# Performance work log

Hardware: AMD Instinct MI355X
Metric: run time of the kernel (lower is better)

Reference implementation:

```python
import jax, jax.numpy as jnp
import numpy as np
import math

# Equal-size graphs make SAGPooling's top-k static; removed edges are kept with a validity mask.
B, N0, D, H, HID, POS, DEG = 64, 400, 128, 4, 64, 16, 16
C = D // H                     # per-head dim = 32
EG = N0 * DEG                  # edges per graph
E = B * EG                     # 409600 edges total
RATIO = 0.8
K1 = math.ceil(RATIO * N0)     # 320
K2 = math.ceil(RATIO * K1)     # 256
K3 = math.ceil(RATIO * K2)     # 205
KS = (K1, K2, K3)
EPS = 1e-5

def _lin(x, W, b):
    return x @ W + b

def _ln(x, g, b):
    mu = x.mean(-1, keepdims=True)
    var = ((x - mu) ** 2).mean(-1, keepdims=True)
    return (x - mu) * jax.lax.rsqrt(var + EPS) * g + b

def _bn(x, g, b):  # BatchNorm1d, training mode (biased batch variance)
    mu = x.mean(0)
    var = ((x - mu) ** 2).mean(0)
    return (x - mu) * jax.lax.rsqrt(var + EPS) * g + b

def _transformer_conv(x, src, dst, mask, Wq, bq, Wk, bk, Wv, bv, Ws, bs, N):
    # PyG TransformerConv (concat=True, root_weight=True): scatter-softmax attention over edges
    q = _lin(x, Wq, bq).reshape(N, H, C)
    k = _lin(x, Wk, bk).reshape(N, H, C)
    v = _lin(x, Wv, bv).reshape(N, H, C)
    logits = jnp.einsum('ehc,ehc->eh', q[dst], k[src]) / jnp.sqrt(jnp.float32(C))
    logits = jnp.where(mask[:, None], logits, -1e9)
    m = jnp.maximum(jax.ops.segment_max(logits, dst, num_segments=N), -1e9)
    w = jnp.exp(logits - m[dst]) * mask[:, None]
    denom = jax.ops.segment_sum(w, dst, num_segments=N)
    alpha = w / jnp.where(denom[dst] > 0, denom[dst], 1.0)  # [E,H]
    msg = jax.ops.segment_sum(v[src] * alpha[:, :, None], dst, num_segments=N)
    return msg.reshape(N, D) + _lin(x, Ws, bs)

def _gt_block(x, src, dst, mask, Wq, bq, Wk, bk, Wv, bv, Ws, bs,
              Wlo, blo, g1, be1, W1, b1, W2, b2, g2, be2, N):
    out1 = _lin(_transformer_conv(x, src, dst, mask, Wq, bq, Wk, bk, Wv, bv, Ws, bs, N), Wlo, blo)
    out2 = _ln(out1 + x, g1, be1)
    out3 = _lin(jax.nn.relu(_lin(out2, W1, b1)), W2, b2)
    return _ln(out3 + out2, g2, be2)

def _sag_pool(x, src, dst, mask, Wrel, brel, Wroot, n, k):
    # SAGPooling: GraphConv(aggr='add') scorer, tanh nonlinearity, per-graph top-k, filter_adj via mask
    Nn = B * n
    agg = jax.ops.segment_sum(x[src] * mask[:, None], dst, num_segments=Nn)
    s = jnp.tanh((agg @ Wrel + brel + x @ Wroot)[:, 0])
    tv, ti = jax.lax.top_k(s.reshape(B, n), k)  # [B,k]
    perm = (ti + jnp.arange(B, dtype=ti.dtype)[:, None] * n).reshape(-1)
    x_new = x[perm] * tv.reshape(-1, 1)
    kept = jnp.zeros(Nn, bool).at[perm].set(True)
    new_id = jnp.zeros(Nn, jnp.int32).at[perm].set(jnp.arange(B * k, dtype=jnp.int32))
    nm = mask & kept[src] & kept[dst]
    return x_new, jnp.where(nm, new_id[src], 0), jnp.where(nm, new_id[dst], 0), nm

def _forward(x, lap_pos_enc, W_pos, b_pos,
             gt_Wq, gt_bq, gt_Wk, gt_bk, gt_Wv, gt_bv, gt_Wskip, gt_bskip,
             gt_Wlo, gt_blo, gt_ln1g, gt_ln1b, gt_W1, gt_b1, gt_W2, gt_b2, gt_ln2g, gt_ln2b,
             pool_Wrel, pool_brel, pool_Wroot,
             hW1, hb1, hW2, hb2, hW3, hb3, bn1g, bn1b, bn2g, bn2b,
             edge_src, edge_dst):
    x = x + _lin(lap_pos_enc, W_pos, b_pos)
    src, dst = edge_src, edge_dst
    mask = jnp.ones(src.shape, bool)
    n = N0
    feats = []
    for i in range(3):
        x = _gt_block(x, src, dst, mask,
                      gt_Wq[i], gt_bq[i], gt_Wk[i], gt_bk[i], gt_Wv[i], gt_bv[i],
                      gt_Wskip[i], gt_bskip[i], gt_Wlo[i], gt_blo[i],
                      gt_ln1g[i], gt_ln1b[i], gt_W1[i], gt_b1[i], gt_W2[i], gt_b2[i],
                      gt_ln2g[i], gt_ln2b[i], B * n)
        x, src, dst, mask = _sag_pool(x, src, dst, mask, pool_Wrel[i], pool_brel[i], pool_Wroot[i], n, KS[i])
        n = KS[i]
        xg = x.reshape(B, n, D)
        feats.append(jnp.concatenate([xg.max(1), xg.mean(1)], axis=1))  # [B, 2D] = gmp | gap
    xf = feats[0] + feats[1] + feats[2]
    h = jax.nn.relu(_bn(_lin(xf, hW1, hb1), bn1g, bn1b))
    h = jax.nn.relu(_bn(_lin(h, hW2, hb2), bn2g, bn2b))
    return _lin(h, hW3, hb3)[:, 0]  # [B]

def setup_inputs():
    key = jax.random.key(0)
    ks = jax.random.split(key, 16)
    rn = lambda k, shape, fan: jax.random.normal(k, shape, jnp.float32) / np.float32(np.sqrt(fan))
    inp = {}
    inp['x'] = jax.random.normal(ks[0], (B * N0, D), jnp.float32)
    inp['lap_pos_enc'] = jax.random.normal(ks[1], (B * N0, POS), jnp.float32)
    offs = (jnp.arange(B, dtype=jnp.int32) * N0)[:, None]
    inp['edge_src'] = (jax.random.randint(ks[2], (B, EG), 0, N0, jnp.int32) + offs).reshape(-1)
    inp['edge_dst'] = (jax.random.randint(ks[3], (B, EG), 0, N0, jnp.int32) + offs).reshape(-1)
    inp['W_pos'] = rn(ks[4], (POS, D), POS); inp['b_pos'] = jnp.zeros(D)
    pk = jax.random.split(ks[5], 12)
    inp['gt_Wq'] = rn(pk[0], (3, D, D), D); inp['gt_bq'] = jnp.zeros((3, D))
    inp['gt_Wk'] = rn(pk[1], (3, D, D), D); inp['gt_bk'] = jnp.zeros((3, D))
    inp['gt_Wv'] = rn(pk[2], (3, D, D), D); inp['gt_bv'] = jnp.zeros((3, D))
    inp['gt_Wskip'] = rn(pk[3], (3, D, D), D); inp['gt_bskip'] = jnp.zeros((3, D))
    inp['gt_Wlo'] = rn(pk[4], (3, D, D), D); inp['gt_blo'] = jnp.zeros((3, D))
    inp['gt_ln1g'] = jnp.ones((3, D)); inp['gt_ln1b'] = jnp.zeros((3, D))
    inp['gt_W1'] = rn(pk[5], (3, D, HID), D); inp['gt_b1'] = jnp.zeros((3, HID))
    inp['gt_W2'] = rn(pk[6], (3, HID, D), HID); inp['gt_b2'] = jnp.zeros((3, D))
    inp['gt_ln2g'] = jnp.ones((3, D)); inp['gt_ln2b'] = jnp.zeros((3, D))
    inp['pool_Wrel'] = rn(pk[7], (3, D, 1), D); inp['pool_brel'] = jnp.zeros((3, 1))
    inp['pool_Wroot'] = rn(pk[8], (3, D, 1), D)
    inp['hW1'] = rn(pk[9], (2 * D, D), 2 * D); inp['hb1'] = jnp.zeros(D)
    inp['hW2'] = rn(pk[10], (D, D // 2), D); inp['hb2'] = jnp.zeros(D // 2)
    inp['hW3'] = rn(pk[11], (D // 2, 1), D // 2); inp['hb3'] = jnp.zeros(1)
    inp['bn1g'] = jnp.ones(D); inp['bn1b'] = jnp.zeros(D)
    inp['bn2g'] = jnp.ones(D // 2); inp['bn2b'] = jnp.zeros(D // 2)
    return inp

def reference(x, lap_pos_enc, edge_src, edge_dst, W_pos, b_pos,
              gt_Wq, gt_bq, gt_Wk, gt_bk, gt_Wv, gt_bv, gt_Wskip, gt_bskip,
              gt_Wlo, gt_blo, gt_ln1g, gt_ln1b, gt_W1, gt_b1, gt_W2, gt_b2, gt_ln2g, gt_ln2b,
              pool_Wrel, pool_brel, pool_Wroot,
              hW1, hb1, hW2, hb2, hW3, hb3, bn1g, bn1b, bn2g, bn2b):
    return _forward(x, lap_pos_enc, W_pos, b_pos,
                    gt_Wq, gt_bq, gt_Wk, gt_bk, gt_Wv, gt_bv, gt_Wskip, gt_bskip,
                    gt_Wlo, gt_blo, gt_ln1g, gt_ln1b, gt_W1, gt_b1, gt_W2, gt_b2, gt_ln2g, gt_ln2b,
                    pool_Wrel, pool_brel, pool_Wroot,
                    hW1, hb1, hW2, hb2, hW3, hb3, bn1g, bn1b, bn2g, bn2b,
                    edge_src, edge_dst)
```

## Files before the change

### kernel.cpp

```cpp
#include <hip/hip_runtime.h>
#include <math.h>

#define BB   64
#define NPG0 400
#define DD   128
#define HH   4
#define CC   32
#define HIDD 64
#define POSD 16
#define EE   409600
#define EG   6400

__global__ void k_pos(const float* __restrict__ x, const float* __restrict__ lap,
                      const float* __restrict__ Wp, const float* __restrict__ bp,
                      float* __restrict__ out, int N){
  __shared__ float W[POSD*DD];
  __shared__ float bsh[DD];
  for(int i=threadIdx.x;i<POSD*DD;i+=blockDim.x) W[i]=Wp[i];
  for(int i=threadIdx.x;i<DD;i+=blockDim.x) bsh[i]=bp[i];
  __syncthreads();
  int total=N*DD;
  for(int idx=blockIdx.x*blockDim.x+threadIdx.x; idx<total; idx+=gridDim.x*blockDim.x){
    int n=idx>>7, d=idx&127;
    const float* lr=lap+(size_t)n*POSD;
    float acc=bsh[d]+x[idx];
    #pragma unroll
    for(int p=0;p<POSD;p++) acc=fmaf(lr[p],W[p*DD+d],acc);
    out[idx]=acc;
  }
}

__global__ __launch_bounds__(512) void k_gemm4_sw(
    const float* __restrict__ X,
    const float* __restrict__ W0,const float* __restrict__ W1,
    const float* __restrict__ W2,const float* __restrict__ W3,
    const float* __restrict__ b0,const float* __restrict__ b1,
    const float* __restrict__ b2,const float* __restrict__ b3,
    float* __restrict__ Y0,float* __restrict__ Y1,
    float* __restrict__ Y2,float* __restrict__ Y3){
  constexpr int XPAD=DD+4;
  __shared__ float Xl[128*XPAD];
  int tid=threadIdx.x;
  { const float4* xs=(const float4*)(X+(size_t)blockIdx.x*128*DD);
    for(int i=tid;i<128*32;i+=512){
      int r=i>>5, kq=i&31;
      *(float4*)&Xl[r*XPAD+kq*4]=xs[i];
    } }
  __syncthreads();
  int lane=tid&63;
  int wv=__builtin_amdgcn_readfirstlane(tid>>6);
  int cbase=wv*16;
  int row0=blockIdx.x*128+lane;
  int row1=row0+64;
  const float* xr0=&Xl[lane*XPAD];
  const float* xr1=&Xl[(lane+64)*XPAD];
  auto one=[&](const float* __restrict__ Wg,const float* __restrict__ bias,float* __restrict__ Y){
    float a0[16],a1[16];
    #pragma unroll
    for(int c=0;c<16;c++){a0[c]=0.f;a1[c]=0.f;}
    #pragma unroll 2
    for(int kt=0;kt<32;kt++){
      float4 xv0=*(const float4*)&xr0[4*kt];
      float4 xv1=*(const float4*)&xr1[4*kt];
      float xk0[4]={xv0.x,xv0.y,xv0.z,xv0.w};
      float xk1[4]={xv1.x,xv1.y,xv1.z,xv1.w};
      #pragma unroll
      for(int kk=0;kk<4;kk++){
        const float4* wrow=(const float4*)(Wg+(size_t)(4*kt+kk)*DD+cbase);
        #pragma unroll
        for(int cg=0;cg<4;cg++){
          float4 w4=wrow[cg];
          a0[cg*4+0]=fmaf(xk0[kk],w4.x,a0[cg*4+0]);
          a0[cg*4+1]=fmaf(xk0[kk],w4.y,a0[cg*4+1]);
          a0[cg*4+2]=fmaf(xk0[kk],w4.z,a0[cg*4+2]);
          a0[cg*4+3]=fmaf(xk0[kk],w4.w,a0[cg*4+3]);
          a1[cg*4+0]=fmaf(xk1[kk],w4.x,a1[cg*4+0]);
          a1[cg*4+1]=fmaf(xk1[kk],w4.y,a1[cg*4+1]);
          a1[cg*4+2]=fmaf(xk1[kk],w4.z,a1[cg*4+2]);
          a1[cg*4+3]=fmaf(xk1[kk],w4.w,a1[cg*4+3]);
        }
      }
    }
    const float4* bb4=(const float4*)(bias+cbase);
    #pragma unroll
    for(int cg=0;cg<4;cg++){
      float4 b4=bb4[cg];
      float4 v0,v1;
      v0.x=a0[cg*4+0]+b4.x; v0.y=a0[cg*4+1]+b4.y;
      v0.z=a0[cg*4+2]+b4.z; v0.w=a0[cg*4+3]+b4.w;
      v1.x=a1[cg*4+0]+b4.x; v1.y=a1[cg*4+1]+b4.y;
      v1.z=a1[cg*4+2]+b4.z; v1.w=a1[cg*4+3]+b4.w;
      *(float4*)&Y[(size_t)row0*DD+cbase+cg*4]=v0;
      *(float4*)&Y[(size_t)row1*DD+cbase+cg*4]=v1;
    }
  };
  one(W0,b0,Y0);
  one(W1,b1,Y1);
  one(W2,b2,Y2);
  one(W3,b3,Y3);
}

__global__ __launch_bounds__(512) void k_ffn_fused(
    const float* __restrict__ Xg, const float* __restrict__ resid,
    const float* __restrict__ Wlo, const float* __restrict__ blo,
    const float* __restrict__ l1g, const float* __restrict__ l1b,
    const float* __restrict__ W1, const float* __restrict__ b1,
    const float* __restrict__ W2, const float* __restrict__ b2,
    const float* __restrict__ l2g, const float* __restrict__ l2b,
    float* __restrict__ Y){
  constexpr int XPAD=DD+4;
  constexpr int HPAD=HIDD+4;
  __shared__ float Xa[64*XPAD];
  __shared__ float hb[64*HPAD];
  __shared__ float redA[8*64];
  __shared__ float redB[8*64];
  int tid=threadIdx.x;
  { const float4* xs=(const float4*)(Xg+(size_t)blockIdx.x*64*DD);
    for(int i=tid;i<64*32;i+=512){
      int r=i>>5, kq=i&31;
      *(float4*)&Xa[r*XPAD+kq*4]=xs[i];
    } }
  __syncthreads();
  int lane=tid&63;
  int wv=__builtin_amdgcn_readfirstlane(tid>>6);
  int row=blockIdx.x*64+lane;
  const float* xr=&Xa[lane*XPAD];

  int cbase=wv*16;
  float acc[16];
  #pragma unroll
  for(int c=0;c<16;c++) acc[c]=0.f;
  #pragma unroll 2
  for(int kt=0;kt<32;kt++){
    float4 xv=*(const float4*)&xr[4*kt];
    float xk[4]={xv.x,xv.y,xv.z,xv.w};
    #pragma unroll
    for(int kk=0;kk<4;kk++){
      const float4* wrow=(const float4*)(Wlo+(size_t)(4*kt+kk)*DD+cbase);
      #pragma unroll
      for(int cg=0;cg<4;cg++){
        float4 w4=wrow[cg];
        acc[cg*4+0]=fmaf(xk[kk],w4.x,acc[cg*4+0]);
        acc[cg*4+1]=fmaf(xk[kk],w4.y,acc[cg*4+1]);
        acc[cg*4+2]=fmaf(xk[kk],w4.z,acc[cg*4+2]);
        acc[cg*4+3]=fmaf(xk[kk],w4.w,acc[cg*4+3]);
      }
    }
  }
  { const float4* bb4=(const float4*)(blo+cbase);
    #pragma unroll
    for(int cg=0;cg<4;cg++){
      float4 b4=bb4[cg];
      float4 rv=*(const float4*)&resid[(size_t)row*DD+cbase+cg*4];
      acc[cg*4+0]+=b4.x+rv.x; acc[cg*4+1]+=b4.y+rv.y;
      acc[cg*4+2]+=b4.z+rv.z; acc[cg*4+3]+=b4.w+rv.w;
    } }
  { float ps=0.f,pq=0.f;
    #pragma unroll
    for(int c=0;c<16;c++){ ps+=acc[c]; pq+=acc[c]*acc[c]; }
    redA[wv*64+lane]=ps; redB[wv*64+lane]=pq;
    __syncthreads();
    float s=0.f,q=0.f;
    #pragma unroll
    for(int w=0;w<8;w++){ s+=redA[w*64+lane]; q+=redB[w*64+lane]; }
    float mu=s*(1.f/DD);
    float inv=1.0f/sqrtf(q*(1.f/DD)-mu*mu+1e-5f);
    const float4* g4p=(const float4*)(l1g+cbase);
    const float4* e4p=(const float4*)(l1b+cbase);
    #pragma unroll
    for(int cg=0;cg<4;cg++){
      float4 g4=g4p[cg], e4=e4p[cg];
      float4 v;
      v.x=(acc[cg*4+0]-mu)*inv*g4.x+e4.x;
      v.y=(acc[cg*4+1]-mu)*inv*g4.y+e4.y;
      v.z=(acc[cg*4+2]-mu)*inv*g4.z+e4.z;
      v.w=(acc[cg*4+3]-mu)*inv*g4.w+e4.w;
      *(float4*)&Xa[lane*XPAD+cbase+cg*4]=v;
    } }
  __syncthreads();

  { int cb2=wv*8;
    float acc2[8];
    #pragma unroll
    for(int c=0;c<8;c++) acc2[c]=0.f;
    #pragma unroll 2
    for(int kt=0;kt<32;kt++){
      float4 xv=*(const float4*)&xr[4*kt];
      float xk[4]={xv.x,xv.y,xv.z,xv.w};
      #pragma unroll
      for(int kk=0;kk<4;kk++){
        const float4* wrow=(const float4*)(W1+(size_t)(4*kt+kk)*HIDD+cb2);
        #pragma unroll
        for(int cg=0;cg<2;cg++){
          float4 w4=wrow[cg];
          acc2[cg*4+0]=fmaf(xk[kk],w4.x,acc2[cg*4+0]);
          acc2[cg*4+1]=fmaf(xk[kk],w4.y,acc2[cg*4+1]);
          acc2[cg*4+2]=fmaf(xk[kk],w4.z,acc2[cg*4+2]);
          acc2[cg*4+3]=fmaf(xk[kk],w4.w,acc2[cg*4+3]);
        }
      }
    }
    const float4* bb4=(const float4*)(b1+cb2);
    #pragma unroll
    for(int cg=0;cg<2;cg++){
      float4 b4=bb4[cg];
      float4 v;
      v.x=fmaxf(acc2[cg*4+0]+b4.x,0.f); v.y=fmaxf(acc2[cg*4+1]+b4.y,0.f);
      v.z=fmaxf(acc2[cg*4+2]+b4.z,0.f); v.w=fmaxf(acc2[cg*4+3]+b4.w,0.f);
      *(float4*)&hb[lane*HPAD+cb2+cg*4]=v;
    } }
  __syncthreads();

  { float acc3[16];
    #pragma unroll
    for(int c=0;c<16;c++) acc3[c]=0.f;
    const float* hr=&hb[lane*HPAD];
    #pragma unroll 2
    for(int kt=0;kt<16;kt++){
      float4 xv=*(const float4*)&hr[4*kt];
      float xk[4]={xv.x,xv.y,xv.z,xv.w};
      #pragma unroll
      for(int kk=0;kk<4;kk++){
        const float4* wrow=(const float4*)(W2+(size_t)(4*kt+kk)*DD+cbase);
        #pragma unroll
        for(int cg=0;cg<4;cg++){
          float4 w4=wrow[cg];
          acc3[cg*4+0]=fmaf(xk[kk],w4.x,acc3[cg*4+0]);
          acc3[cg*4+1]=fmaf(xk[kk],w4.y,acc3[cg*4+1]);
          acc3[cg*4+2]=fmaf(xk[kk],w4.z,acc3[cg*4+2]);
          acc3[cg*4+3]=fmaf(xk[kk],w4.w,acc3[cg*4+3]);
        }
      }
    }
    const float4* bb4=(const float4*)(b2+cbase);
    #pragma unroll
    for(int cg=0;cg<4;cg++){
      float4 b4=bb4[cg];
      float4 rv=*(const float4*)&Xa[lane*XPAD+cbase+cg*4];
      acc3[cg*4+0]+=b4.x+rv.x; acc3[cg*4+1]+=b4.y+rv.y;
      acc3[cg*4+2]+=b4.z+rv.z; acc3[cg*4+3]+=b4.w+rv.w;
    }
    float ps=0.f,pq=0.f;
    #pragma unroll
    for(int c=0;c<16;c++){ ps+=acc3[c]; pq+=acc3[c]*acc3[c]; }
    __syncthreads();
    redA[wv*64+lane]=ps; redB[wv*64+lane]=pq;
    __syncthreads();
    float s=0.f,q=0.f;
    #pragma unroll
    for(int w=0;w<8;w++){ s+=redA[w*64+lane]; q+=redB[w*64+lane]; }
    float mu=s*(1.f/DD);
    float inv=1.0f/sqrtf(q*(1.f/DD)-mu*mu+1e-5f);
    const float4* g4p=(const float4*)(l2g+cbase);
    const float4* e4p=(const float4*)(l2b+cbase);
    #pragma unroll
    for(int cg=0;cg<4;cg++){
      float4 g4=g4p[cg], e4=e4p[cg];
      float4 v;
      v.x=(acc3[cg*4+0]-mu)*inv*g4.x+e4.x;
      v.y=(acc3[cg*4+1]-mu)*inv*g4.y+e4.y;
      v.z=(acc3[cg*4+2]-mu)*inv*g4.z+e4.z;
      v.w=(acc3[cg*4+3]-mu)*inv*g4.w+e4.w;
      *(float4*)&Y[(size_t)row*DD+cbase+cg*4]=v;
    } }
}

__global__ __launch_bounds__(512) void k_csr(const int* __restrict__ src,const int* __restrict__ dst,
   const int* __restrict__ msk,const int* __restrict__ kept,const int* __restrict__ nid,int n,
   int* __restrict__ rowstart,int* __restrict__ rowcnt,int* __restrict__ esrc,
   int* __restrict__ nsrc,int* __restrict__ ndst,int* __restrict__ nmsk){
  __shared__ int cnt[512];
  __shared__ int woff[512];
  int b=blockIdx.x, t=threadIdx.x;
  cnt[t]=0;
  __syncthreads();
  int ebase=b*EG, nbase=b*n;
  for(int j=t;j<EG;j+=512){
    int e=ebase+j;
    int s,d,m;
    if(kept){
      int s0=src[e], d0=dst[e];
      m=(msk?msk[e]:1) && kept[s0] && kept[d0];
      s=m?nid[s0]:0; d=m?nid[d0]:0;
      nsrc[e]=s; ndst[e]=d; nmsk[e]=m;
    } else { s=src[e]; d=dst[e]; m=1; }
    if(m) atomicAdd(&cnt[d-nbase],1);
  }
  __syncthreads();
  int v=cnt[t];
  woff[t]=v;
  __syncthreads();
  for(int off=1;off<512;off<<=1){
    int a=(t>=off)?woff[t-off]:0;
    __syncthreads();
    woff[t]+=a;
    __syncthreads();
  }
  int excl=woff[t]-v;
  if(t<n){ rowstart[nbase+t]=ebase+excl; rowcnt[nbase+t]=v; }
  __syncthreads();
  woff[t]=excl;
  __syncthreads();
  for(int j=t;j<EG;j+=512){
    int e=ebase+j;
    int s,d,m;
    if(kept){ m=nmsk[e]; s=nsrc[e]; d=ndst[e]; }
    else { m=1; s=src[e]; d=dst[e]; }
    if(!m) continue;
    int off=atomicAdd(&woff[d-nbase],1);
    esrc[ebase+off]=s;
  }
}

template<int NG>
__global__ __launch_bounds__(512) void k_attn4(const float* __restrict__ q,const float* __restrict__ kk,
     const float* __restrict__ v,const int* __restrict__ rowstart,const int* __restrict__ rowcnt,
     const int* __restrict__ esrc,float* __restrict__ attn){
  __shared__ float4 kl[NG*9];
  __shared__ float4 vl[NG*9];
  int b=blockIdx.x>>2, h=blockIdx.x&3;
  int nb=b*NG;
  const float4* kg=(const float4*)kk;
  const float4* vg=(const float4*)v;
  for(int i=threadIdx.x;i<NG*8;i+=512){
    int node=i>>3, qq=i&7;
    size_t gidx=(size_t)(nb+node)*32 + h*8 + qq;
    kl[node*9+qq]=kg[gidx];
    vl[node*9+qq]=vg[gidx];
  }
  __syncthreads();
  int node=threadIdx.x;
  if(node>=NG) return;
  int gn=nb+node;
  float4 q0,q1,q2,q3,q4,q5,q6,q7;
  { const float4* qp=(const float4*)(q+(size_t)gn*DD+h*CC);
    q0=qp[0];q1=qp[1];q2=qp[2];q3=qp[3];q4=qp[4];q5=qp[5];q6=qp[6];q7=qp[7]; }
  int st=rowstart[gn], cn=rowcnt[gn];
  float m=-1e30f, s=0.f;
  float4 o0={0,0,0,0},o1={0,0,0,0},o2={0,0,0,0},o3={0,0,0,0};
  float4 o4={0,0,0,0},o5={0,0,0,0},o6={0,0,0,0},o7={0,0,0,0};
  for(int j=0;j<cn;j++){
    int sl=esrc[st+j]-nb;
    const float4* kr=&kl[sl*9];
    float4 k0=kr[0],k1=kr[1],k2=kr[2],k3=kr[3],k4=kr[4],k5=kr[5],k6=kr[6],k7=kr[7];
    float a0=q0.x*k0.x+q0.y*k0.y+q0.z*k0.z+q0.w*k0.w;
    float a1=q1.x*k1.x+q1.y*k1.y+q1.z*k1.z+q1.w*k1.w;
    float a2=q2.x*k2.x+q2.y*k2.y+q2.z*k2.z+q2.w*k2.w;
    float a3=q3.x*k3.x+q3.y*k3.y+q3.z*k3.z+q3.w*k3.w;
    a0+=q4.x*k4.x+q4.y*k4.y+q4.z*k4.z+q4.w*k4.w;
    a1+=q5.x*k5.x+q5.y*k5.y+q5.z*k5.z+q5.w*k5.w;
    a2+=q6.x*k6.x+q6.y*k6.y+q6.z*k6.z+q6.w*k6.w;
    a3+=q7.x*k7.x+q7.y*k7.y+q7.z*k7.z+q7.w*k7.w;
    float lg=((a0+a1)+(a2+a3))*0.17677669529663687f;
    const float4* vr=&vl[sl*9];
    float4 v0=vr[0],v1=vr[1],v2=vr[2],v3=vr[3],v4=vr[4],v5=vr[5],v6=vr[6],v7=vr[7];
    if(lg<=m){
      float w=__expf(lg-m);
      s+=w;
      o0.x=fmaf(w,v0.x,o0.x);o0.y=fmaf(w,v0.y,o0.y);o0.z=fmaf(w,v0.z,o0.z);o0.w=fmaf(w,v0.w,o0.w);
      o1.x=fmaf(w,v1.x,o1.x);o1.y=fmaf(w,v1.y,o1.y);o1.z=fmaf(w,v1.z,o1.z);o1.w=fmaf(w,v1.w,o1.w);
      o2.x=fmaf(w,v2.x,o2.x);o2.y=fmaf(w,v2.y,o2.y);o2.z=fmaf(w,v2.z,o2.z);o2.w=fmaf(w,v2.w,o2.w);
      o3.x=fmaf(w,v3.x,o3.x);o3.y=fmaf(w,v3.y,o3.y);o3.z=fmaf(w,v3.z,o3.z);o3.w=fmaf(w,v3.w,o3.w);
      o4.x=fmaf(w,v4.x,o4.x);o4.y=fmaf(w,v4.y,o4.y);o4.z=fmaf(w,v4.z,o4.z);o4.w=fmaf(w,v4.w,o4.w);
      o5.x=fmaf(w,v5.x,o5.x);o5.y=fmaf(w,v5.y,o5.y);o5.z=fmaf(w,v5.z,o5.z);o5.w=fmaf(w,v5.w,o5.w);
      o6.x=fmaf(w,v6.x,o6.x);o6.y=fmaf(w,v6.y,o6.y);o6.z=fmaf(w,v6.z,o6.z);o6.w=fmaf(w,v6.w,o6.w);
      o7.x=fmaf(w,v7.x,o7.x);o7.y=fmaf(w,v7.y,o7.y);o7.z=fmaf(w,v7.z,o7.z);o7.w=fmaf(w,v7.w,o7.w);
    } else {
      float r=__expf(m-lg);
      s=fmaf(s,r,1.f);
      o0.x=fmaf(o0.x,r,v0.x);o0.y=fmaf(o0.y,r,v0.y);o0.z=fmaf(o0.z,r,v0.z);o0.w=fmaf(o0.w,r,v0.w);
      o1.x=fmaf(o1.x,r,v1.x);o1.y=fmaf(o1.y,r,v1.y);o1.z=fmaf(o1.z,r,v1.z);o1.w=fmaf(o1.w,r,v1.w);
      o2.x=fmaf(o2.x,r,v2.x);o2.y=fmaf(o2.y,r,v2.y);o2.z=fmaf(o2.z,r,v2.z);o2.w=fmaf(o2.w,r,v2.w);
      o3.x=fmaf(o3.x,r,v3.x);o3.y=fmaf(o3.y,r,v3.y);o3.z=fmaf(o3.z,r,v3.z);o3.w=fmaf(o3.w,r,v3.w);
      o4.x=fmaf(o4.x,r,v4.x);o4.y=fmaf(o4.y,r,v4.y);o4.z=fmaf(o4.z,r,v4.z);o4.w=fmaf(o4.w,r,v4.w);
      o5.x=fmaf(o5.x,r,v5.x);o5.y=fmaf(o5.y,r,v5.y);o5.z=fmaf(o5.z,r,v5.z);o5.w=fmaf(o5.w,r,v5.w);
      o6.x=fmaf(o6.x,r,v6.x);o6.y=fmaf(o6.y,r,v6.y);o6.z=fmaf(o6.z,r,v6.z);o6.w=fmaf(o6.w,r,v6.w);
      o7.x=fmaf(o7.x,r,v7.x);o7.y=fmaf(o7.y,r,v7.y);o7.z=fmaf(o7.z,r,v7.z);o7.w=fmaf(o7.w,r,v7.w);
      m=lg;
    }
  }
  float inv=(s>0.f)?(1.f/s):0.f;
  float* op=attn+(size_t)gn*DD+h*CC;
  float4* op4=(float4*)op;
  float4 r0=op4[0],r1=op4[1],r2=op4[2],r3=op4[3],r4=op4[4],r5=op4[5],r6=op4[6],r7=op4[7];
  r0.x+=o0.x*inv;r0.y+=o0.y*inv;r0.z+=o0.z*inv;r0.w+=o0.w*inv;
  r1.x+=o1.x*inv;r1.y+=o1.y*inv;r1.z+=o1.z*inv;r1.w+=o1.w*inv;
  r2.x+=o2.x*inv;r2.y+=o2.y*inv;r2.z+=o2.z*inv;r2.w+=o2.w*inv;
  r3.x+=o3.x*inv;r3.y+=o3.y*inv;r3.z+=o3.z*inv;r3.w+=o3.w*inv;
  r4.x+=o4.x*inv;r4.y+=o4.y*inv;r4.z+=o4.z*inv;r4.w+=o4.w*inv;
  r5.x+=o5.x*inv;r5.y+=o5.y*inv;r5.z+=o5.z*inv;r5.w+=o5.w*inv;
  r6.x+=o6.x*inv;r6.y+=o6.y*inv;r6.z+=o6.z*inv;r6.w+=o6.w*inv;
  r7.x+=o7.x*inv;r7.y+=o7.y*inv;r7.z+=o7.z*inv;r7.w+=o7.w*inv;
  op4[0]=r0;op4[1]=r1;op4[2]=r2;op4[3]=r3;op4[4]=r4;op4[5]=r5;op4[6]=r6;op4[7]=r7;
}

__global__ __launch_bounds__(512) void k_sagtopk(const float* __restrict__ x,
   const float* __restrict__ wrel,const float* __restrict__ wroot,const float* __restrict__ brel,
   const int* __restrict__ rowstart,const int* __restrict__ rowcnt,const int* __restrict__ esrc,
   int n,int k,float* __restrict__ tv,int* __restrict__ gi,
   int* __restrict__ kept,int* __restrict__ nid){
  __shared__ float pnl[NPG0];
  __shared__ float sv[512];
  __shared__ int   si[512];
  int b=blockIdx.x, t=threadIdx.x, nbase=b*n;
  float rdot=0.f;
  if(t<n){
    const float4* xr=(const float4*)(x+(size_t)(nbase+t)*DD);
    float p=0.f;
    #pragma unroll
    for(int qq=0;qq<32;qq++){
      float4 xv=xr[qq];
      float4 wr=((const float4*)wrel)[qq];
      float4 wo=((const float4*)wroot)[qq];
      p   =fmaf(xv.x,wr.x,fmaf(xv.y,wr.y,fmaf(xv.z,wr.z,fmaf(xv.w,wr.w,p))));
      rdot=fmaf(xv.x,wo.x,fmaf(xv.y,wo.y,fmaf(xv.z,wo.z,fmaf(xv.w,wo.w,rdot))));
    }
    pnl[t]=p;
  }
  __syncthreads();
  float sc=-INFINITY;
  if(t<n){
    int st=rowstart[nbase+t], cn=rowcnt[nbase+t];
    float s=0.f;
    for(int j=0;j<cn;j++) s+=pnl[esrc[st+j]-nbase];
    sc=tanhf(s+brel[0]+rdot);
  }
  sv[t]=(t<n)?sc:-INFINITY;
  si[t]=t;
  for(int ksz=2;ksz<=512;ksz<<=1){
    for(int j=ksz>>1;j>0;j>>=1){
      __syncthreads();
      int ixj=t^j;
      if(ixj>t){
        float s1=sv[t], s2=sv[ixj];
        int i1=si[t], i2=si[ixj];
        bool firstRanks=(s1>s2)||(s1==s2&&i1<i2);
        bool up=((t&ksz)==0);
        if(up? !firstRanks : firstRanks){ sv[t]=s2;sv[ixj]=s1;si[t]=i2;si[ixj]=i1; }
      }
    }
  }
  __syncthreads();
  if(t<k){
    int oldg=nbase+si[t];
    tv[b*k+t]=sv[t];
    gi[b*k+t]=oldg;
    kept[oldg]=1;
    nid[oldg]=b*k+t;
  } else if(t<n){
    kept[nbase+si[t]]=0;
  }
}

__global__ void k_gather(const float* __restrict__ xin, const int* __restrict__ gi,
                         const float* __restrict__ tv, float* __restrict__ xout, int rows){
  int idx=blockIdx.x*blockDim.x+threadIdx.x;
  if(idx>=rows*DD) return;
  int r=idx>>7;
  int d=idx&127;
  xout[idx]=xin[(size_t)gi[r]*DD+d]*tv[r];
}

__global__ __launch_bounds__(512) void k_readout(const float* __restrict__ xk, int k,
                                                 float* __restrict__ xf){
  __shared__ float pm[512];
  __shared__ float ps[512];
  int b=blockIdx.x, t=threadIdx.x;
  int d=t&127, strip=t>>7;
  const float* base=xk+((size_t)b*k)*DD+d;
  float mx=-INFINITY, sm=0.f;
  for(int j=strip;j<k;j+=4){
    float v=base[(size_t)j*DD];
    mx=fmaxf(mx,v); sm+=v;
  }
  pm[t]=mx; ps[t]=sm;
  __syncthreads();
  if(t<128){
    float m0=fmaxf(fmaxf(pm[t],pm[t+128]),fmaxf(pm[t+256],pm[t+384]));
    float s0=ps[t]+ps[t+128]+ps[t+256]+ps[t+384];
    xf[b*256+t]+=m0;
    xf[b*256+128+t]+=s0/(float)k;
  }
}

__global__ void k_h1(const float* __restrict__ xf,const float* __restrict__ W,const float* __restrict__ b,float* __restrict__ z){
  int i=blockIdx.x*blockDim.x+threadIdx.x; if(i>=BB*DD) return;
  int r=i>>7, j=i&127;
  float acc=b[j];
  const float* xr=xf+r*256;
  #pragma unroll 8
  for(int t=0;t<256;t++) acc=fmaf(xr[t], W[t*DD+j], acc);
  z[i]=acc;
}
__global__ void k_bnrelu(const float* __restrict__ z,const float* __restrict__ g,const float* __restrict__ be,
                         float* __restrict__ h,int cols){
  int j=blockIdx.x*blockDim.x+threadIdx.x; if(j>=cols) return;
  float mu=0.f;
  for(int r=0;r<BB;r++) mu+=z[r*cols+j];
  mu*=(1.f/BB);
  float var=0.f;
  for(int r=0;r<BB;r++){ float d=z[r*cols+j]-mu; var+=d*d; }
  var*=(1.f/BB);
  float inv=1.0f/sqrtf(var+1e-5f);
  float gg=g[j], bb=be[j];
  for(int r=0;r<BB;r++){ float y=(z[r*cols+j]-mu)*inv*gg+bb; h[r*cols+j]=fmaxf(y,0.f); }
}
__global__ void k_h2(const float* __restrict__ h1,const float* __restrict__ W,const float* __restrict__ b,float* __restrict__ z){
  int i=blockIdx.x*blockDim.x+threadIdx.x; if(i>=BB*HIDD) return;
  int r=i>>6, j=i&63;
  float acc=b[j];
  #pragma unroll 8
  for(int t=0;t<DD;t++) acc=fmaf(h1[r*DD+t], W[t*HIDD+j], acc);
  z[i]=acc;
}
__global__ void k_h3(const float* __restrict__ h2,const float* __restrict__ W,const float* __restrict__ b,float* __restrict__ out){
  int bi=threadIdx.x; if(bi>=BB) return;
  float acc=b[0];
  for(int t=0;t<HIDD;t++) acc=fmaf(h2[bi*HIDD+t], W[t], acc);
  out[bi]=acc;
}

extern "C" void kernel_launch(void* const* d_in, const int* in_sizes, int n_in,
                              void* d_out, int out_size, void* d_ws, size_t ws_size,
                              hipStream_t stream){
  (void)in_sizes; (void)n_in; (void)out_size; (void)ws_size;
  const float* x_in =(const float*)d_in[0];
  const float* lap  =(const float*)d_in[1];
  const int*   esrc0=(const int*)  d_in[2];
  const int*   edst0=(const int*)  d_in[3];
  const float* Wpos =(const float*)d_in[4];
  const float* bpos =(const float*)d_in[5];
  const float* gWq  =(const float*)d_in[6];
  const float* gbq  =(const float*)d_in[7];
  const float* gWk  =(const float*)d_in[8];
  const float* gbk  =(const float*)d_in[9];
  const float* gWv  =(const float*)d_in[10];
  const float* gbv  =(const float*)d_in[11];
  const float* gWs  =(const float*)d_in[12];
  const float* gbs  =(const float*)d_in[13];
  const float* gWlo =(const float*)d_in[14];
  const float* gblo =(const float*)d_in[15];
  const float* gl1g =(const float*)d_in[16];
  const float* gl1b =(const float*)d_in[17];
  const float* gW1  =(const float*)d_in[18];
  const float* gb1  =(const float*)d_in[19];
  const float* gW2  =(const float*)d_in[20];
  const float* gb2  =(const float*)d_in[21];
  const float* gl2g =(const float*)d_in[22];
  const float* gl2b =(const float*)d_in[23];
  const float* pWrel=(const float*)d_in[24];
  const float* pbrel=(const float*)d_in[25];
  const float* pWrt =(const float*)d_in[26];
  const float* hW1  =(const float*)d_in[27];
  const float* hb1  =(const float*)d_in[28];
  const float* hW2  =(const float*)d_in[29];
  const float* hb2  =(const float*)d_in[30];
  const float* hW3  =(const float*)d_in[31];
  const float* hb3  =(const float*)d_in[32];
  const float* bn1g =(const float*)d_in[33];
  const float* bn1b =(const float*)d_in[34];
  const float* bn2g =(const float*)d_in[35];
  const float* bn2b =(const float*)d_in[36];
  float* out=(float*)d_out;

  char* base=(char*)d_ws; size_t off=0;
  auto alloc=[&](size_t bytes)->void*{ void* p=base+off; off+=(bytes+255)&~(size_t)255; return p; };
  const int NMAX=BB*NPG0;
  float* xA  =(float*)alloc((size_t)NMAX*DD*4);
  float* qb  =(float*)alloc((size_t)NMAX*DD*4);
  float* kb  =(float*)alloc((size_t)NMAX*DD*4);
  float* vb  =(float*)alloc((size_t)NMAX*DD*4);
  float* xO  =(float*)alloc((size_t)NMAX*DD*4);
  int*   rowstart=(int*)alloc((size_t)NMAX*4);
  int*   rowcnt  =(int*)alloc((size_t)NMAX*4);
  int*   esrcW   =(int*)alloc((size_t)EE*4);
  float* tvb =(float*)alloc((size_t)BB*320*4);
  int*   gib =(int*)  alloc((size_t)BB*320*4);
  int*   kept=(int*)  alloc((size_t)NMAX*4);
  int*   nid =(int*)  alloc((size_t)NMAX*4);
  int*   srcA=(int*)  alloc((size_t)EE*4);
  int*   dstA=(int*)  alloc((size_t)EE*4);
  int*   mskA=(int*)  alloc((size_t)EE*4);
  int*   srcB=(int*)  alloc((size_t)EE*4);
  int*   dstB=(int*)  alloc((size_t)EE*4);
  int*   mskB=(int*)  alloc((size_t)EE*4);
  float* xf  =(float*)alloc((size_t)BB*256*4);
  float* z1  =(float*)alloc((size_t)BB*DD*4);
  float* h1b =(float*)alloc((size_t)BB*DD*4);
  float* z2  =(float*)alloc((size_t)BB*HIDD*4);
  float* h2b =(float*)alloc((size_t)BB*HIDD*4);

  const int npg[3]={400,320,256};
  const int kpg[3]={320,256,205};
  const int Nin[3]={BB*400, BB*320, BB*256};

  hipMemsetAsync(xf,0,(size_t)BB*256*4,stream);
  k_pos<<<2048,256,0,stream>>>(x_in,lap,Wpos,bpos,xA,Nin[0]);

  const int* src=esrc0; const int* dst=edst0; const int* msk=nullptr;

  for(int i=0;i<3;i++){
    int N=Nin[i];
    int gB=N/64;
    int gB2=N/128;
    const float* Wq=gWq+(size_t)i*DD*DD;   const float* bq=gbq+(size_t)i*DD;
    const float* Wk=gWk+(size_t)i*DD*DD;   const float* bk=gbk+(size_t)i*DD;
    const float* Wv=gWv+(size_t)i*DD*DD;   const float* bv=gbv+(size_t)i*DD;
    const float* Ws=gWs+(size_t)i*DD*DD;   const float* bs=gbs+(size_t)i*DD;
    const float* Wlo=gWlo+(size_t)i*DD*DD; const float* blo=gblo+(size_t)i*DD;
    const float* l1g=gl1g+(size_t)i*DD;    const float* l1b=gl1b+(size_t)i*DD;
    const float* W1=gW1+(size_t)i*DD*HIDD; const float* b1=gb1+(size_t)i*HIDD;
    const float* W2=gW2+(size_t)i*HIDD*DD; const float* b2=gb2+(size_t)i*DD;
    const float* l2g=gl2g+(size_t)i*DD;    const float* l2b=gl2b+(size_t)i*DD;
    const float* wrel=pWrel+(size_t)i*DD;  const float* brel=pbrel+(size_t)i;
    const float* wrt=pWrt+(size_t)i*DD;

    if(i==0){
      k_csr<<<BB,512,0,stream>>>(src,dst,nullptr,nullptr,nullptr,npg[i],
                                 rowstart,rowcnt,esrcW,nullptr,nullptr,nullptr);
    } else {
      int* ns=(i==1)?srcA:srcB; int* ndd=(i==1)?dstA:dstB; int* nm=(i==1)?mskA:mskB;
      k_csr<<<BB,512,0,stream>>>(src,dst,msk,kept,nid,npg[i],
                                 rowstart,rowcnt,esrcW,ns,ndd,nm);
      src=ns; dst=ndd; msk=nm;
    }

    k_gemm4_sw<<<gB2,512,0,stream>>>(xA,Wq,Wk,Wv,Ws,bq,bk,bv,bs,qb,kb,vb,xO);
    if(i==0)      k_attn4<400><<<BB*HH,512,0,stream>>>(qb,kb,vb,rowstart,rowcnt,esrcW,xO);
    else if(i==1) k_attn4<320><<<BB*HH,512,0,stream>>>(qb,kb,vb,rowstart,rowcnt,esrcW,xO);
    else          k_attn4<256><<<BB*HH,512,0,stream>>>(qb,kb,vb,rowstart,rowcnt,esrcW,xO);
    k_ffn_fused<<<gB,512,0,stream>>>(xO,xA,Wlo,blo,l1g,l1b,W1,b1,W2,b2,l2g,l2b,xO);

    k_sagtopk<<<BB,512,0,stream>>>(xO,wrel,wrt,brel,rowstart,rowcnt,esrcW,
                                   npg[i],kpg[i],tvb,gib,kept,nid);
    int rows=BB*kpg[i];
    k_gather<<<(rows*DD+255)/256,256,0,stream>>>(xO,gib,tvb,xA,rows);
    k_readout<<<BB,512,0,stream>>>(xA,kpg[i],xf);
  }

  k_h1<<<(BB*DD+127)/128,128,0,stream>>>(xf,hW1,hb1,z1);
  k_bnrelu<<<1,128,0,stream>>>(z1,bn1g,bn1b,h1b,DD);
  k_h2<<<(BB*HIDD+127)/128,128,0,stream>>>(h1b,hW2,hb2,z2);
  k_bnrelu<<<1,64,0,stream>>>(z2,bn2g,bn2b,h2b,HIDD);
  k_h3<<<1,64,0,stream>>>(h2b,hW3,hb3,out);
}
```

Measured before the change: 580.2 us.

## Restructure QKV/skip GEMM to column-per-lane tiling with all four outputs fused

Replaces the LDS-staged GEMM, where each wave owned 16 columns and 2 rows and ran the four projections one after another, with a register-only kernel. Each lane now owns 2 columns, and each wave 8 rows, across all four weight matrices at once. X rows are read as wave-uniform broadcasts straight from global memory, and weight rows are read coalesced as float2. This drops the shared-memory staging and barrier and reuses each X value across four outputs, at the cost of 64 accumulators per lane and twice as many blocks. Register pressure under the 512-thread launch bound and the uncached broadcast X loads may limit the gain.

```diff
diff --git a/kernel.cpp b/kernel.cpp
--- a/kernel.cpp
+++ b/kernel.cpp
@@ -30,7 +30,7 @@
   }
 }
 
-__global__ __launch_bounds__(512) void k_gemm4_sw(
+__global__ __launch_bounds__(512) void k_gemm4_cw(
     const float* __restrict__ X,
     const float* __restrict__ W0,const float* __restrict__ W1,
     const float* __restrict__ W2,const float* __restrict__ W3,
@@ -38,66 +38,62 @@
     const float* __restrict__ b2,const float* __restrict__ b3,
     float* __restrict__ Y0,float* __restrict__ Y1,
     float* __restrict__ Y2,float* __restrict__ Y3){
-  constexpr int XPAD=DD+4;
-  __shared__ float Xl[128*XPAD];
   int tid=threadIdx.x;
-  { const float4* xs=(const float4*)(X+(size_t)blockIdx.x*128*DD);
-    for(int i=tid;i<128*32;i+=512){
-      int r=i>>5, kq=i&31;
-      *(float4*)&Xl[r*XPAD+kq*4]=xs[i];
-    } }
-  __syncthreads();
   int lane=tid&63;
   int wv=__builtin_amdgcn_readfirstlane(tid>>6);
-  int cbase=wv*16;
-  int row0=blockIdx.x*128+lane;
-  int row1=row0+64;
-  const float* xr0=&Xl[lane*XPAD];
-  const float* xr1=&Xl[(lane+64)*XPAD];
-  auto one=[&](const float* __restrict__ Wg,const float* __restrict__ bias,float* __restrict__ Y){
-    float a0[16],a1[16];
-    #pragma unroll
-    for(int c=0;c<16;c++){a0[c]=0.f;a1[c]=0.f;}
-    #pragma unroll 2
-    for(int kt=0;kt<32;kt++){
-      float4 xv0=*(const float4*)&xr0[4*kt];
-      float4 xv1=*(const float4*)&xr1[4*kt];
-      float xk0[4]={xv0.x,xv0.y,xv0.z,xv0.w};
-      float xk1[4]={xv1.x,xv1.y,xv1.z,xv1.w};
+  int rbase=blockIdx.x*64+wv*8;
+  int c0=lane*2;
+  float aQ[16],aK[16],aV[16],aS[16];
+  #pragma unroll
+  for(int i=0;i<16;i++){aQ[i]=0.f;aK[i]=0.f;aV[i]=0.f;aS[i]=0.f;}
+  const float* Xb=X+(size_t)rbase*DD;
+  for(int kt=0;kt<32;kt++){
+    float4 xs0=*(const float4*)(Xb+0*DD+4*kt);
+    float4 xs1=*(const float4*)(Xb+1*DD+4*kt);
+    float4 xs2=*(const float4*)(Xb+2*DD+4*kt);
+    float4 xs3=*(const float4*)(Xb+3*DD+4*kt);
+    float4 xs4=*(const float4*)(Xb+4*DD+4*kt);
+    float4 xs5=*(const float4*)(Xb+5*DD+4*kt);
+    float4 xs6=*(const float4*)(Xb+6*DD+4*kt);
+    float4 xs7=*(const float4*)(Xb+7*DD+4*kt);
+    #pragma unroll
+    for(int kk=0;kk<4;kk++){
+      size_t woff=(size_t)(4*kt+kk)*DD+c0;
+      float2 wq=*(const float2*)(W0+woff);
+      float2 wk=*(const float2*)(W1+woff);
+      float2 wvv=*(const float2*)(W2+woff);
+      float2 ws=*(const float2*)(W3+woff);
+      float x0=(kk==0)?xs0.x:(kk==1)?xs0.y:(kk==2)?xs0.z:xs0.w;
+      float x1=(kk==0)?xs1.x:(kk==1)?xs1.y:(kk==2)?xs1.z:xs1.w;
+      float x2=(kk==0)?xs2.x:(kk==1)?xs2.y:(kk==2)?xs2.z:xs2.w;
+      float x3=(kk==0)?xs3.x:(kk==1)?xs3.y:(kk==2)?xs3.z:xs3.w;
+      float x4=(kk==0)?xs4.x:(kk==1)?xs4.y:(kk==2)?xs4.z:xs4.w;
+      float x5=(kk==0)?xs5.x:(kk==1)?xs5.y:(kk==2)?xs5.z:xs5.w;
+      float x6=(kk==0)?xs6.x:(kk==1)?xs6.y:(kk==2)?xs6.z:xs6.w;
+      float x7=(kk==0)?xs7.x:(kk==1)?xs7.y:(kk==2)?xs7.z:xs7.w;
+      float xr[8]={x0,x1,x2,x3,x4,x5,x6,x7};
       #pragma unroll
-      for(int kk=0;kk<4;kk++){
-        const float4* wrow=(const float4*)(Wg+(size_t)(4*kt+kk)*DD+cbase);
-        #pragma unroll
-        for(int cg=0;cg<4;cg++){
-          float4 w4=wrow[cg];
-          a0[cg*4+0]=fmaf(xk0[kk],w4.x,a0[cg*4+0]);
-          a0[cg*4+1]=fmaf(xk0[kk],w4.y,a0[cg*4+1]);
-          a0[cg*4+2]=fmaf(xk0[kk],w4.z,a0[cg*4+2]);
-          a0[cg*4+3]=fmaf(xk0[kk],w4.w,a0[cg*4+3]);
-          a1[cg*4+0]=fmaf(xk1[kk],w4.x,a1[cg*4+0]);
-          a1[cg*4+1]=fmaf(xk1[kk],w4.y,a1[cg*4+1]);
-          a1[cg*4+2]=fmaf(xk1[kk],w4.z,a1[cg*4+2]);
-          a1[cg*4+3]=fmaf(xk1[kk],w4.w,a1[cg*4+3]);
-        }
+      for(int r=0;r<8;r++){
+        aQ[r*2+0]=fmaf(xr[r],wq.x, aQ[r*2+0]); aQ[r*2+1]=fmaf(xr[r],wq.y, aQ[r*2+1]);
+        aK[r*2+0]=fmaf(xr[r],wk.x, aK[r*2+0]); aK[r*2+1]=fmaf(xr[r],wk.y, aK[r*2+1]);
+        aV[r*2+0]=fmaf(xr[r],wvv.x,aV[r*2+0]); aV[r*2+1]=fmaf(xr[r],wvv.y,aV[r*2+1]);
+        aS[r*2+0]=fmaf(xr[r],ws.x, aS[r*2+0]); aS[r*2+1]=fmaf(xr[r],ws.y, aS[r*2+1]);
       }
     }
-    const float4* bb4=(const float4*)(bias+cbase);
-    #pragma unroll
-    for(int cg=0;cg<4;cg++){
-      float4 b4=bb4[cg];
-      float4 v0,v1;
-      v0.x=a0[cg*4+0]+b4.x; v0.y=a0[cg*4+1]+b4.y;
-      v0.z=a0[cg*4+2]+b4.z; v0.w=a0[cg*4+3]+b4.w;
-      v1.x=a1[cg*4+0]+b4.x; v1.y=a1[cg*4+1]+b4.y;
-      v1.z=a1[cg*4+2]+b4.z; v1.w=a1[cg*4+3]+b4.w;
-      *(float4*)&Y[(size_t)row0*DD+cbase+cg*4]=v0;
-      *(float4*)&Y[(size_t)row1*DD+cbase+cg*4]=v1;
-    }
-  };
-  one(W0,b0,Y0);
-  one(W1,b1,Y1);
-  one(W2,b2,Y2);
-  one(W3,b3,Y3);
+  }
+  float2 bq=*(const float2*)(b0+c0);
+  float2 bk=*(const float2*)(b1+c0);
+  float2 bv=*(const float2*)(b2+c0);
+  float2 bs=*(const float2*)(b3+c0);
+  #pragma unroll
+  for(int r=0;r<8;r++){
+    size_t yo=(size_t)(rbase+r)*DD+c0;
+    float2 v;
+    v.x=aQ[r*2]+bq.x; v.y=aQ[r*2+1]+bq.y; *(float2*)(Y0+yo)=v;
+    v.x=aK[r*2]+bk.x; v.y=aK[r*2+1]+bk.y; *(float2*)(Y1+yo)=v;
+    v.x=aV[r*2]+bv.x; v.y=aV[r*2+1]+bv.y; *(float2*)(Y2+yo)=v;
+    v.x=aS[r*2]+bs.x; v.y=aS[r*2+1]+bs.y; *(float2*)(Y3+yo)=v;
+  }
 }
 
 __global__ __launch_bounds__(512) void k_ffn_fused(
@@ -602,7 +598,6 @@
   for(int i=0;i<3;i++){
     int N=Nin[i];
     int gB=N/64;
-    int gB2=N/128;
     const float* Wq=gWq+(size_t)i*DD*DD;   const float* bq=gbq+(size_t)i*DD;
     const float* Wk=gWk+(size_t)i*DD*DD;   const float* bk=gbk+(size_t)i*DD;
     const float* Wv=gWv+(size_t)i*DD*DD;   const float* bv=gbv+(size_t)i*DD;
@@ -625,7 +620,7 @@
       src=ns; dst=ndd; msk=nm;
     }
 
-    k_gemm4_sw<<<gB2,512,0,stream>>>(xA,Wq,Wk,Wv,Ws,bq,bk,bv,bs,qb,kb,vb,xO);
+    k_gemm4_cw<<<gB,512,0,stream>>>(xA,Wq,Wk,Wv,Ws,bq,bk,bv,bs,qb,kb,vb,xO);
     if(i==0)      k_attn4<400><<<BB*HH,512,0,stream>>>(qb,kb,vb,rowstart,rowcnt,esrcW,xO);
     else if(i==1) k_attn4<320><<<BB*HH,512,0,stream>>>(qb,kb,vb,rowstart,rowcnt,esrcW,xO);
     else          k_attn4<256><<<BB*HH,512,0,stream>>>(qb,kb,vb,rowstart,rowcnt,esrcW,xO);
```

New measurement: 589.5 us. About the same (+1.6%).
